# Kernel optimization log

Measured on AMD Instinct MI355X. Metric: run time of the kernel, lower is better.

The kernel has to match this reference:

```python
import jax, jax.numpy as jnp
import numpy as np

B, T = 16, 2048
N_PROBLEMS, N_KCS, N_HIDDEN = 10000, 64, 128


def setup_inputs() -> dict:
    key = jax.random.key(0)
    ks = jax.random.split(key, 9)
    y = (jax.random.uniform(ks[0], (B, T)) > 0.5).astype(jnp.float32)  # binary responses
    problem_seq = jax.random.randint(ks[1], (B, T), 0, N_PROBLEMS)
    # soft assignment matrix (rows roughly on the simplex, like gumbel_softmax output)
    A = jax.nn.softmax(jax.random.normal(ks[2], (N_PROBLEMS, N_KCS)), axis=1)
    kc_embd_w = jax.random.normal(ks[3], (N_KCS, N_HIDDEN)) * 0.1
    lam_w = jax.random.normal(ks[4], (N_HIDDEN, 1)) * 0.02
    lam_b = jnp.zeros((1,), jnp.float32)
    guess_w = jax.random.normal(ks[5], (N_HIDDEN, 1)) * 0.1
    guess_b = jnp.zeros((1,), jnp.float32)
    slip_w = jax.random.normal(ks[6], (N_HIDDEN, 1)) * 0.1
    slip_b = jnp.zeros((1,), jnp.float32)
    return {"y": y, "problem_seq": problem_seq, "A": A,
            "kc_embd_w": kc_embd_w, "lam_w": lam_w, "lam_b": lam_b,
            "guess_w": guess_w, "guess_b": guess_b,
            "slip_w": slip_w, "slip_b": slip_b}


def reference(y, problem_seq, A, kc_embd_w, lam_w, lam_b, guess_w, guess_b, slip_w, slip_b):
    x = A[problem_seq]                                   # [B,T,K]
    sim = jnp.einsum('btk,bsk->bts', x, x)               # [B,T,T]
    t = sim.shape[1]
    mask = jnp.tril(jnp.ones((t, t), sim.dtype), k=-1)   # strictly past
    sim = sim * mask
    # reversed cumsum along last axis: cumsum from the right
    delta_t = jnp.flip(jnp.cumsum(jnp.flip(sim, axis=2), axis=2), axis=2)
    kc = x @ kc_embd_w                                   # [B,T,H]
    kc_lam = jnp.exp(kc @ lam_w + lam_b)                 # [B,T,1]
    weight = sim * jnp.exp(-kc_lam * delta_t)            # [B,T,T]
    weight_normed = weight / (jnp.sum(weight, axis=2, keepdims=True) + 1e-6)
    h = jnp.sum(y[:, None, :] * weight_normed, axis=2)   # [B,T]
    guess = jax.nn.sigmoid(kc @ guess_w + guess_b)[:, :, 0]
    slip = jax.nn.sigmoid(kc @ slip_w + slip_b)[:, :, 0]
    yhat = h * (1 - slip) + (1 - h) * guess
    return jnp.clip(yhat, 0.01, 0.99)
```

## Files before the change

### kernel.cpp

```cpp
#include <hip/hip_runtime.h>

#define B_ 16
#define T_ 2048
#define NP 10000
#define NH 128

#define XF_F   0
#define NLAM_F 1048576
#define GG_F   1081344
#define SS_F   1114112

typedef __attribute__((ext_vector_type(8))) _Float16 f16x8;
typedef __attribute__((ext_vector_type(4))) float f32x4;

__device__ __forceinline__ size_t xfbase(int b, int R, int ks) {
  return (((size_t)b * 128 + R) * 2 + ks) * 512;
}

__global__ __launch_bounds__(256) void prep(
    const int* __restrict__ pseq, const float* __restrict__ A,
    const float* __restrict__ kcw,
    const float* __restrict__ lam_w, const float* __restrict__ lam_b,
    const float* __restrict__ guess_w, const float* __restrict__ guess_b,
    const float* __restrict__ slip_w, const float* __restrict__ slip_b,
    float* __restrict__ ws) {
  const int tid = threadIdx.x, bid = blockIdx.x;
  const int lane = tid & 63, wv = tid >> 6;
  __shared__ float wvec[3][64];
  if (tid < 192) {
    int vec = tid >> 6, k = tid & 63;
    const float* wvp = (vec == 0) ? lam_w : (vec == 1 ? guess_w : slip_w);
    float acc = 0.f;
    #pragma unroll 8
    for (int h = 0; h < NH; ++h) acc = fmaf(kcw[k * NH + h], wvp[h], acc);
    wvec[vec][k] = acc;
  }
  {
    const int W = bid * 4 + wv;
    const int b = W >> 8, rem = W & 255, R = rem >> 1, ks = rem & 1;
    const int row = (R << 4) + (lane & 15), gp = lane >> 4;
    const float* src = A + (size_t)pseq[b * T_ + row] * 64 + ks * 32 + gp * 8;
    float4 v0 = *(const float4*)src;
    float4 v1 = *(const float4*)(src + 4);
    float vv[8] = {v0.x, v0.y, v0.z, v0.w, v1.x, v1.y, v1.z, v1.w};
    union { _Float16 h[8]; f16x8 v; } H;
    #pragma unroll
    for (int i = 0; i < 8; ++i) H.h[i] = (_Float16)vv[i];
    *(f16x8*)((unsigned short*)ws + xfbase(b, R, ks) + lane * 8) = H.v;
  }
  __syncthreads();
  if (tid < 32) {
    const int tg = bid * 32 + tid;
    const float* xr = A + ((size_t)pseq[tg] << 6);
    float aL = 0.f, aG = 0.f, aS = 0.f;
    #pragma unroll
    for (int k = 0; k < 64; ++k) {
      float xv = xr[k];
      aL = fmaf(xv, wvec[0][k], aL);
      aG = fmaf(xv, wvec[1][k], aG);
      aS = fmaf(xv, wvec[2][k], aS);
    }
    ws[NLAM_F + tg] = -__expf(aL + lam_b[0]);
    ws[GG_F + tg]   = 1.f / (1.f + __expf(-(aG + guess_b[0])));
    ws[SS_F + tg]   = 1.f / (1.f + __expf(-(aS + slip_b[0])));
  }
}

__global__ __launch_bounds__(256, 3) void mainK(
    const float* __restrict__ y, float* __restrict__ ws,
    float* __restrict__ out) {
  __shared__ float part[4][3][64];
  const int tid = threadIdx.x, bid = blockIdx.x;
  const int lane = tid & 63;
  const int wv = __builtin_amdgcn_readfirstlane(tid >> 6);
  const int u = bid & 255, half = bid >> 8;
  const int b = u >> 4, kk = u & 15;
  const int tile = half ? kk : 31 - kk;
  const int t0 = tile << 6, base = b * T_;
  const int c = lane & 15, g = lane >> 4;
  const unsigned short* X = (const unsigned short*)ws;

  float nl[4];
  #pragma unroll
  for (int fj = 0; fj < 4; ++fj) nl[fj] = ws[NLAM_F + base + t0 + 16 * fj + c];

  f16x8 bfr[2][2][2];
  #pragma unroll
  for (int fjh = 0; fjh < 2; ++fjh)
    #pragma unroll
    for (int j2 = 0; j2 < 2; ++j2)
      #pragma unroll
      for (int ks = 0; ks < 2; ++ks)
        bfr[fjh][j2][ks] = *(const f16x8*)(X + xfbase(b, tile * 4 + 2 * fjh + j2, ks) + lane * 8);

  const int nchunks = tile + 1;
  const int nc = (nchunks + 3) >> 2;
  const int cLo = wv * nc;
  const int cHi = min(cLo + nc, nchunks);

  float NA[4] = {0,0,0,0}, DA[4] = {0,0,0,0}, RA[4] = {0,0,0,0};

  for (int cc = cHi - 1; cc >= cLo; --cc) {
    const bool diag = (cc == tile);
    float yy[4][4];
    #pragma unroll
    for (int fi = 0; fi < 4; ++fi) {
      float4 t4 = *(const float4*)(y + base + (cc << 6) + 16 * fi + 4 * g);
      yy[fi][0] = t4.x; yy[fi][1] = t4.y; yy[fi][2] = t4.z; yy[fi][3] = t4.w;
    }
    #pragma unroll
    for (int fjh = 0; fjh < 2; ++fjh) {
      f32x4 acc[4][2] = {};
      #pragma unroll
      for (int ks = 0; ks < 2; ++ks) {
        f16x8 afr[4];
        #pragma unroll
        for (int fi = 0; fi < 4; ++fi)
          afr[fi] = *(const f16x8*)(X + xfbase(b, cc * 4 + fi, ks) + lane * 8);
        #pragma unroll
        for (int fi = 0; fi < 4; ++fi)
          #pragma unroll
          for (int j2 = 0; j2 < 2; ++j2)
            acc[fi][j2] = __builtin_amdgcn_mfma_f32_16x16x32_f16(afr[fi], bfr[fjh][j2][ks], acc[fi][j2], 0, 0, 0);
      }
      #pragma unroll
      for (int j2 = 0; j2 < 2; ++j2) {
        const int fj = 2 * fjh + j2;
        float S[4], ft[4];
        #pragma unroll
        for (int fi = 0; fi < 4; ++fi) {
          f32x4 v = acc[fi][j2];
          if (diag) {
            #pragma unroll
            for (int rr = 0; rr < 4; ++rr)
              if (16 * fi + 4 * g + rr >= 16 * fj + c) v[rr] = 0.f;
          }
          const float p0 = ((v.x + v.y) + (v.z + v.w));
          const float u16 = __shfl_xor(p0, 16);
          const float pr = p0 + u16;
          const float u32 = __shfl_xor(pr, 32);
          ft[fi] = pr + u32;
          S[fi] = ((g & 1) ? 0.f : u16) + ((g < 2) ? u32 : 0.f);
        }
        const float F2 = ft[3], F1 = F2 + ft[2], F0 = F1 + ft[1];
        const float Fv[4] = {F0, F1, F2, 0.f};
        float num = 0.f, den = 0.f;
        #pragma unroll
        for (int fi = 0; fi < 4; ++fi) {
          f32x4 v = acc[fi][j2];
          if (diag) {
            #pragma unroll
            for (int rr = 0; rr < 4; ++rr)
              if (16 * fi + 4 * g + rr >= 16 * fj + c) v[rr] = 0.f;
          }
          const float SF = S[fi] + Fv[fi];
          float p3 = v.w, p2 = p3 + v.z, p1 = p2 + v.y, p0 = p1 + v.x;
          const float pp[4] = {p0, p1, p2, p3};
          const float sm[4] = {v.x, v.y, v.z, v.w};
          #pragma unroll
          for (int rr = 0; rr < 4; ++rr) {
            const float e = __expf(nl[fj] * (pp[rr] + SF));
            const float w = sm[rr] * e;
            den += w;
            num = fmaf(yy[fi][rr], w, num);
          }
        }
        num += __shfl_xor(num, 16); num += __shfl_xor(num, 32);
        den += __shfl_xor(den, 16); den += __shfl_xor(den, 32);
        const float tot = Fv[0] + ft[0];
        const float e = __expf(nl[fj] * RA[fj]);
        NA[fj] = fmaf(num, e, NA[fj]);
        DA[fj] = fmaf(den, e, DA[fj]);
        RA[fj] += tot;
      }
    }
  }

  if (g == 0) {
    #pragma unroll
    for (int fj = 0; fj < 4; ++fj) {
      part[wv][0][16 * fj + c] = NA[fj];
      part[wv][1][16 * fj + c] = DA[fj];
      part[wv][2][16 * fj + c] = RA[fj];
    }
  }
  __syncthreads();

  if (wv == 0) {
    const int t = t0 + lane;
    const float nlt = ws[NLAM_F + base + t];
    float N = 0.f, D = 0.f, Roff = 0.f;
    #pragma unroll
    for (int w = 3; w >= 0; --w) {
      const float e = __expf(nlt * Roff);
      N = fmaf(part[w][0][lane], e, N);
      D = fmaf(part[w][1][lane], e, D);
      Roff += part[w][2][lane];
    }
    const float gv = ws[GG_F + base + t];
    const float sv = ws[SS_F + base + t];
    const float h = N / (D + 1e-6f);
    float yh = h * (1.f - sv) + (1.f - h) * gv;
    out[base + t] = fminf(fmaxf(yh, 0.01f), 0.99f);
  }
}

extern "C" void kernel_launch(void* const* d_in, const int* in_sizes, int n_in,
                              void* d_out, int out_size, void* d_ws, size_t ws_size,
                              hipStream_t stream) {
  const float* y    = (const float*)d_in[0];
  const int*   pseq = (const int*)  d_in[1];
  const float* A    = (const float*)d_in[2];
  const float* kcw  = (const float*)d_in[3];
  const float* lw   = (const float*)d_in[4];
  const float* lb   = (const float*)d_in[5];
  const float* gw   = (const float*)d_in[6];
  const float* gb   = (const float*)d_in[7];
  const float* sw   = (const float*)d_in[8];
  const float* sb   = (const float*)d_in[9];
  float* out = (float*)d_out;
  float* ws  = (float*)d_ws;

  prep<<<1024, 256, 0, stream>>>(pseq, A, kcw, lw, lb, gw, gb, sw, sb, ws);
  mainK<<<512, 256, 0, stream>>>(y, ws, out);
}
```

Baseline: 136.0 us.

## Split causal tile work into per-chunk wave items with separate reduction kernel

Each wave now handles one (tile, chunk) pair of the lower-triangular block grid, with the pair recovered from a flat triangular index. Partial numerator, denominator and total-similarity values go to global workspace instead of being accumulated across chunks in registers. A new phase2 kernel folds the chunk partials per tile, applying the exponential decay offsets, and writes the output. This is meant to balance the triangular workload evenly across the GPU instead of giving uneven chunk ranges to the four waves of a block. In exchange it adds a third kernel launch, a global round trip for the partials, and reloads of the B fragments for every item.

Result: faster. 121.0 us (-11.0%).

```diff
diff --git a/kernel.cpp b/kernel.cpp
--- a/kernel.cpp
+++ b/kernel.cpp
@@ -4,11 +4,14 @@
 #define T_ 2048
 #define NP 10000
 #define NH 128
+#define ITEMS_PER_B 528
+#define N_ITEMS (B_ * ITEMS_PER_B)
 
 #define XF_F   0
 #define NLAM_F 1048576
 #define GG_F   1081344
 #define SS_F   1114112
+#define PART_F 1146880
 
 typedef __attribute__((ext_vector_type(8))) _Float16 f16x8;
 typedef __attribute__((ext_vector_type(4))) float f32x4;
@@ -66,143 +69,137 @@
   }
 }
 
-__global__ __launch_bounds__(256, 3) void mainK(
-    const float* __restrict__ y, float* __restrict__ ws,
-    float* __restrict__ out) {
-  __shared__ float part[4][3][64];
-  const int tid = threadIdx.x, bid = blockIdx.x;
+__global__ __launch_bounds__(256, 3) void mainF(
+    const float* __restrict__ y, float* __restrict__ ws) {
+  const int tid = threadIdx.x;
   const int lane = tid & 63;
   const int wv = __builtin_amdgcn_readfirstlane(tid >> 6);
-  const int u = bid & 255, half = bid >> 8;
-  const int b = u >> 4, kk = u & 15;
-  const int tile = half ? kk : 31 - kk;
+  const int item = blockIdx.x * 4 + wv;
+  const int b = item / ITEMS_PER_B;
+  const int r0 = item - b * ITEMS_PER_B;
+  int tile = (int)((sqrtf(8.f * (float)r0 + 1.f) - 1.f) * 0.5f);
+  while ((tile + 1) * (tile + 2) / 2 <= r0) ++tile;
+  while (tile * (tile + 1) / 2 > r0) --tile;
+  const int chunk = r0 - tile * (tile + 1) / 2;
   const int t0 = tile << 6, base = b * T_;
   const int c = lane & 15, g = lane >> 4;
+  const bool diag = (chunk == tile);
   const unsigned short* X = (const unsigned short*)ws;
 
   float nl[4];
   #pragma unroll
   for (int fj = 0; fj < 4; ++fj) nl[fj] = ws[NLAM_F + base + t0 + 16 * fj + c];
 
-  f16x8 bfr[2][2][2];
-  #pragma unroll
-  for (int fjh = 0; fjh < 2; ++fjh)
-    #pragma unroll
-    for (int j2 = 0; j2 < 2; ++j2)
-      #pragma unroll
-      for (int ks = 0; ks < 2; ++ks)
-        bfr[fjh][j2][ks] = *(const f16x8*)(X + xfbase(b, tile * 4 + 2 * fjh + j2, ks) + lane * 8);
-
-  const int nchunks = tile + 1;
-  const int nc = (nchunks + 3) >> 2;
-  const int cLo = wv * nc;
-  const int cHi = min(cLo + nc, nchunks);
-
-  float NA[4] = {0,0,0,0}, DA[4] = {0,0,0,0}, RA[4] = {0,0,0,0};
-
-  for (int cc = cHi - 1; cc >= cLo; --cc) {
-    const bool diag = (cc == tile);
-    float yy[4][4];
-    #pragma unroll
-    for (int fi = 0; fi < 4; ++fi) {
-      float4 t4 = *(const float4*)(y + base + (cc << 6) + 16 * fi + 4 * g);
-      yy[fi][0] = t4.x; yy[fi][1] = t4.y; yy[fi][2] = t4.z; yy[fi][3] = t4.w;
-    }
-    #pragma unroll
-    for (int fjh = 0; fjh < 2; ++fjh) {
-      f32x4 acc[4][2] = {};
-      #pragma unroll
-      for (int ks = 0; ks < 2; ++ks) {
-        f16x8 afr[4];
+  f16x8 bfr[4][2];
+  #pragma unroll
+  for (int j = 0; j < 4; ++j)
+    #pragma unroll
+    for (int ks = 0; ks < 2; ++ks)
+      bfr[j][ks] = *(const f16x8*)(X + xfbase(b, tile * 4 + j, ks) + lane * 8);
+
+  float yy[4][4];
+  #pragma unroll
+  for (int fi = 0; fi < 4; ++fi) {
+    float4 t4 = *(const float4*)(y + base + (chunk << 6) + 16 * fi + 4 * g);
+    yy[fi][0] = t4.x; yy[fi][1] = t4.y; yy[fi][2] = t4.z; yy[fi][3] = t4.w;
+  }
+
+  float NUM[4], DEN[4], TOT[4];
+  #pragma unroll
+  for (int fjh = 0; fjh < 2; ++fjh) {
+    f32x4 acc[4][2] = {};
+    #pragma unroll
+    for (int ks = 0; ks < 2; ++ks) {
+      f16x8 afr[4];
+      #pragma unroll
+      for (int fi = 0; fi < 4; ++fi)
+        afr[fi] = *(const f16x8*)(X + xfbase(b, chunk * 4 + fi, ks) + lane * 8);
+      #pragma unroll
+      for (int fi = 0; fi < 4; ++fi)
         #pragma unroll
-        for (int fi = 0; fi < 4; ++fi)
-          afr[fi] = *(const f16x8*)(X + xfbase(b, cc * 4 + fi, ks) + lane * 8);
+        for (int j2 = 0; j2 < 2; ++j2)
+          acc[fi][j2] = __builtin_amdgcn_mfma_f32_16x16x32_f16(afr[fi], bfr[2 * fjh + j2][ks], acc[fi][j2], 0, 0, 0);
+    }
+    #pragma unroll
+    for (int j2 = 0; j2 < 2; ++j2) {
+      const int fj = 2 * fjh + j2;
+      float S[4], ft[4];
+      #pragma unroll
+      for (int fi = 0; fi < 4; ++fi) {
+        f32x4 v = acc[fi][j2];
+        if (diag) {
+          #pragma unroll
+          for (int rr = 0; rr < 4; ++rr)
+            if (16 * fi + 4 * g + rr >= 16 * fj + c) v[rr] = 0.f;
+        }
+        const float p0 = ((v.x + v.y) + (v.z + v.w));
+        const float u16 = __shfl_xor(p0, 16);
+        const float pr = p0 + u16;
+        const float u32 = __shfl_xor(pr, 32);
+        ft[fi] = pr + u32;
+        S[fi] = ((g & 1) ? 0.f : u16) + ((g < 2) ? u32 : 0.f);
+      }
+      const float F2 = ft[3], F1 = F2 + ft[2], F0 = F1 + ft[1];
+      const float Fv[4] = {F0, F1, F2, 0.f};
+      float num = 0.f, den = 0.f;
+      #pragma unroll
+      for (int fi = 0; fi < 4; ++fi) {
+        f32x4 v = acc[fi][j2];
+        if (diag) {
+          #pragma unroll
+          for (int rr = 0; rr < 4; ++rr)
+            if (16 * fi + 4 * g + rr >= 16 * fj + c) v[rr] = 0.f;
+        }
+        const float SF = S[fi] + Fv[fi];
+        float p3 = v.w, p2 = p3 + v.z, p1 = p2 + v.y, p0 = p1 + v.x;
+        const float pp[4] = {p0, p1, p2, p3};
+        const float sm[4] = {v.x, v.y, v.z, v.w};
         #pragma unroll
-        for (int fi = 0; fi < 4; ++fi)
-          #pragma unroll
-          for (int j2 = 0; j2 < 2; ++j2)
-            acc[fi][j2] = __builtin_amdgcn_mfma_f32_16x16x32_f16(afr[fi], bfr[fjh][j2][ks], acc[fi][j2], 0, 0, 0);
+        for (int rr = 0; rr < 4; ++rr) {
+          const float e = __expf(nl[fj] * (pp[rr] + SF));
+          const float w = sm[rr] * e;
+          den += w;
+          num = fmaf(yy[fi][rr], w, num);
+        }
       }
-      #pragma unroll
-      for (int j2 = 0; j2 < 2; ++j2) {
-        const int fj = 2 * fjh + j2;
-        float S[4], ft[4];
-        #pragma unroll
-        for (int fi = 0; fi < 4; ++fi) {
-          f32x4 v = acc[fi][j2];
-          if (diag) {
-            #pragma unroll
-            for (int rr = 0; rr < 4; ++rr)
-              if (16 * fi + 4 * g + rr >= 16 * fj + c) v[rr] = 0.f;
-          }
-          const float p0 = ((v.x + v.y) + (v.z + v.w));
-          const float u16 = __shfl_xor(p0, 16);
-          const float pr = p0 + u16;
-          const float u32 = __shfl_xor(pr, 32);
-          ft[fi] = pr + u32;
-          S[fi] = ((g & 1) ? 0.f : u16) + ((g < 2) ? u32 : 0.f);
-        }
-        const float F2 = ft[3], F1 = F2 + ft[2], F0 = F1 + ft[1];
-        const float Fv[4] = {F0, F1, F2, 0.f};
-        float num = 0.f, den = 0.f;
-        #pragma unroll
-        for (int fi = 0; fi < 4; ++fi) {
-          f32x4 v = acc[fi][j2];
-          if (diag) {
-            #pragma unroll
-            for (int rr = 0; rr < 4; ++rr)
-              if (16 * fi + 4 * g + rr >= 16 * fj + c) v[rr] = 0.f;
-          }
-          const float SF = S[fi] + Fv[fi];
-          float p3 = v.w, p2 = p3 + v.z, p1 = p2 + v.y, p0 = p1 + v.x;
-          const float pp[4] = {p0, p1, p2, p3};
-          const float sm[4] = {v.x, v.y, v.z, v.w};
-          #pragma unroll
-          for (int rr = 0; rr < 4; ++rr) {
-            const float e = __expf(nl[fj] * (pp[rr] + SF));
-            const float w = sm[rr] * e;
-            den += w;
-            num = fmaf(yy[fi][rr], w, num);
-          }
-        }
-        num += __shfl_xor(num, 16); num += __shfl_xor(num, 32);
-        den += __shfl_xor(den, 16); den += __shfl_xor(den, 32);
-        const float tot = Fv[0] + ft[0];
-        const float e = __expf(nl[fj] * RA[fj]);
-        NA[fj] = fmaf(num, e, NA[fj]);
-        DA[fj] = fmaf(den, e, DA[fj]);
-        RA[fj] += tot;
-      }
-    }
-  }
-
+      num += __shfl_xor(num, 16); num += __shfl_xor(num, 32);
+      den += __shfl_xor(den, 16); den += __shfl_xor(den, 32);
+      NUM[fj] = num; DEN[fj] = den; TOT[fj] = Fv[0] + ft[0];
+    }
+  }
+  float* po = ws + PART_F + (size_t)item * 192;
   if (g == 0) {
     #pragma unroll
     for (int fj = 0; fj < 4; ++fj) {
-      part[wv][0][16 * fj + c] = NA[fj];
-      part[wv][1][16 * fj + c] = DA[fj];
-      part[wv][2][16 * fj + c] = RA[fj];
-    }
-  }
-  __syncthreads();
-
-  if (wv == 0) {
-    const int t = t0 + lane;
-    const float nlt = ws[NLAM_F + base + t];
-    float N = 0.f, D = 0.f, Roff = 0.f;
-    #pragma unroll
-    for (int w = 3; w >= 0; --w) {
-      const float e = __expf(nlt * Roff);
-      N = fmaf(part[w][0][lane], e, N);
-      D = fmaf(part[w][1][lane], e, D);
-      Roff += part[w][2][lane];
-    }
-    const float gv = ws[GG_F + base + t];
-    const float sv = ws[SS_F + base + t];
-    const float h = N / (D + 1e-6f);
-    float yh = h * (1.f - sv) + (1.f - h) * gv;
-    out[base + t] = fminf(fmaxf(yh, 0.01f), 0.99f);
-  }
+      po[16 * fj + c] = NUM[fj];
+      po[64 + 16 * fj + c] = DEN[fj];
+      po[128 + 16 * fj + c] = TOT[fj];
+    }
+  }
+}
+
+__global__ __launch_bounds__(256) void phase2(
+    const float* __restrict__ ws, float* __restrict__ out) {
+  const int tid = threadIdx.x;
+  const int lane = tid & 63;
+  const int widx = blockIdx.x * 4 + (tid >> 6);
+  const int b = widx >> 5, tile = widx & 31;
+  const int t = (tile << 6) + lane, base = b * T_;
+  const float nlt = ws[NLAM_F + base + t];
+  const int ibase = b * ITEMS_PER_B + tile * (tile + 1) / 2;
+  float N = 0.f, D = 0.f, Roff = 0.f;
+  for (int cc = tile; cc >= 0; --cc) {
+    const float* p = ws + PART_F + (size_t)(ibase + cc) * 192;
+    const float e = __expf(nlt * Roff);
+    N = fmaf(p[lane], e, N);
+    D = fmaf(p[64 + lane], e, D);
+    Roff += p[128 + lane];
+  }
+  const float gv = ws[GG_F + base + t];
+  const float sv = ws[SS_F + base + t];
+  const float h = N / (D + 1e-6f);
+  float yh = h * (1.f - sv) + (1.f - h) * gv;
+  out[base + t] = fminf(fmaxf(yh, 0.01f), 0.99f);
 }
 
 extern "C" void kernel_launch(void* const* d_in, const int* in_sizes, int n_in,
@@ -222,5 +219,6 @@
   float* ws  = (float*)d_ws;
 
   prep<<<1024, 256, 0, stream>>>(pseq, A, kcw, lw, lb, gw, gb, sw, sb, ws);
-  mainK<<<512, 256, 0, stream>>>(y, ws, out);
-}
+  mainF<<<N_ITEMS / 4, 256, 0, stream>>>(y, ws);
+  phase2<<<128, 256, 0, stream>>>(ws, out);
+}
```
